# Kernel optimization log

Measured on AMD Instinct MI355X. Metric: run time of the kernel, lower is better.

Reference implementation:

```python
import jax, jax.numpy as jnp
import numpy as np

N_QUBITS = 8
N_LAYERS = 4
N_WIRES = N_QUBITS + 1  # circuit uses an extra ancilla wire
B = 16384
D = 512
LN_EPS = 1e-5


def _rx(theta):
    # RX(t) = [[cos(t/2), -i sin(t/2)], [-i sin(t/2), cos(t/2)]]; theta: () or (B,)
    c = jnp.cos(theta / 2).astype(jnp.complex64)
    s = (-1j) * jnp.sin(theta / 2).astype(jnp.complex64)
    return jnp.stack([jnp.stack([c, s], -1), jnp.stack([s, c], -1)], -2)


def _ry(theta):
    c = jnp.cos(theta / 2).astype(jnp.complex64)
    s = jnp.sin(theta / 2).astype(jnp.complex64)
    return jnp.stack([jnp.stack([c, -s], -1), jnp.stack([s, c], -1)], -2)


def _rz(theta):
    # RZ(t) = diag(e^{-it/2}, e^{it/2})
    half = (theta / 2).astype(jnp.complex64)
    em = jnp.exp(-1j * half)
    ep = jnp.exp(1j * half)
    z = jnp.zeros_like(em)
    return jnp.stack([jnp.stack([em, z], -1), jnp.stack([z, ep], -1)], -2)


def _apply_1q(state, U, wire):
    # state: (B,) + (2,)*N_WIRES ; U: (2,2) shared or (B,2,2) per-sample
    ax = 1 + wire
    s = jnp.moveaxis(state, ax, -1)
    if U.ndim == 2:
        s = jnp.einsum('ij,...j->...i', U, s)
    else:
        s = jnp.einsum('bij,b...j->b...i', U, s)
    return jnp.moveaxis(s, -1, ax)


def _cnot(state, c, t):
    # flip target wire t on the control=1 slice of wire c
    s = jnp.moveaxis(state, (1 + c, 1 + t), (-2, -1))
    s = jnp.stack([s[..., 0, :], jnp.flip(s[..., 1, :], axis=-1)], axis=-2)
    return jnp.moveaxis(s, (-2, -1), (1 + c, 1 + t))


def _quantum_circuit(angles, q_weights):
    # angles: (B, N_QUBITS) per-sample data angles; q_weights: (N_LAYERS, N_QUBITS+1)
    b = angles.shape[0]
    state = jnp.zeros((b, 2 ** N_WIRES), jnp.complex64).at[:, 0].set(1.0)
    state = state.reshape((b,) + (2,) * N_WIRES)
    # data encoding: RX, RZ with per-sample angles
    for i in range(N_QUBITS):
        state = _apply_1q(state, _rx(angles[:, i]), i)
        state = _apply_1q(state, _rz(angles[:, i]), i)
    # first variational layer
    for i in range(N_QUBITS):
        state = _apply_1q(state, _rx(q_weights[0, i]), i)
        state = _apply_1q(state, _rz(q_weights[1, i]), i)
    # entangling layers
    for l in range(1, N_LAYERS):
        for i in range(N_QUBITS):
            state = _cnot(state, i, (i + 1) % N_QUBITS)
            state = _apply_1q(state, _ry(q_weights[l, i]), i)
            state = _apply_1q(state, _rz(q_weights[l, i]), i)
        state = _cnot(state, N_QUBITS - 1, N_QUBITS)
        state = _apply_1q(state, _ry(q_weights[l, -1]), N_QUBITS)
    probs = state.real ** 2 + state.imag ** 2
    # <Z_i> = P(q_i=0) - P(q_i=1)
    zs = []
    for i in range(N_QUBITS):
        axes = tuple(1 + j for j in range(N_WIRES) if j != i)
        p = probs.sum(axes)  # (B, 2)
        zs.append(p[:, 0] - p[:, 1])
    return jnp.stack(zs, axis=1)  # (B, N_QUBITS)


def _forward(x, timestep, w_in, b_in, ln_gamma, ln_beta, q_weights, w_out, b_out):
    h = jnp.tanh(x @ w_in.T + b_in)  # (B, 8)
    mu = h.mean(-1, keepdims=True)
    var = ((h - mu) ** 2).mean(-1, keepdims=True)
    h = (h - mu) / jnp.sqrt(var + LN_EPS) * ln_gamma + ln_beta
    angles = h + timestep  # broadcast scalar timestep
    q_out = _quantum_circuit(angles, q_weights)
    out = q_out @ w_out.T + b_out
    return x + out  # input_dim == output_dim -> residual


def setup_inputs() -> dict:
    key = jax.random.key(0)
    ks = jax.random.split(key, 6)
    x = jax.random.normal(ks[0], (B, D), jnp.float32)
    timestep = jax.random.uniform(ks[1], (1,), jnp.float32)
    w_in = jax.random.normal(ks[2], (N_QUBITS, D), jnp.float32) * np.float32(1.0 / np.sqrt(D))
    b_in = jnp.zeros((N_QUBITS,), jnp.float32)
    ln_gamma = jnp.ones((N_QUBITS,), jnp.float32)
    ln_beta = jnp.zeros((N_QUBITS,), jnp.float32)
    q_weights = jax.random.uniform(ks[3], (N_LAYERS, N_QUBITS + 1), jnp.float32, 0.0, 2.0 * np.pi)
    w_out = jax.random.normal(ks[4], (D, N_QUBITS), jnp.float32) * np.float32(1.0 / np.sqrt(N_QUBITS))
    b_out = jnp.zeros((D,), jnp.float32)
    return {'x': x, 'timestep': timestep, 'w_in': w_in, 'b_in': b_in,
            'ln_gamma': ln_gamma, 'ln_beta': ln_beta, 'q_weights': q_weights,
            'w_out': w_out, 'b_out': b_out}


def reference(x, timestep, w_in, b_in, ln_gamma, ln_beta, q_weights, w_out, b_out):
    return _forward(x, timestep, w_in, b_in, ln_gamma, ln_beta, q_weights, w_out, b_out)
```

## Files before the change

### kernel.cpp

```cpp
#include <hip/hip_runtime.h>
#include <math.h>

#define NSAMP 16384
#define ND    512

typedef float f2 __attribute__((ext_vector_type(2)));
__device__ __forceinline__ f2 spl(float x) { return (f2){x, x}; }

template<int CTRL>
__device__ __forceinline__ float dppf(float x) {
  return __int_as_float(__builtin_amdgcn_update_dpp(
      __float_as_int(x), __float_as_int(x), CTRL, 0xF, 0xF, true));
}
template<int CTRL, int RM, int BM>
__device__ __forceinline__ float dppf_keep(float x) {
  return __int_as_float(__builtin_amdgcn_update_dpp(
      __float_as_int(x), __float_as_int(x), CTRL, RM, BM, false));
}
template<int P>
__device__ __forceinline__ float swzf(float x) {
  return __int_as_float(__builtin_amdgcn_ds_swizzle(__float_as_int(x), P));
}

#if __has_builtin(__builtin_amdgcn_permlane16_swap)
#define HAVE_PLSWAP 1
#endif
__device__ __forceinline__ void plswap16(float x, float& a, float& b) {
#ifdef HAVE_PLSWAP
  auto r = __builtin_amdgcn_permlane16_swap(__float_as_uint(x), __float_as_uint(x), false, false);
  a = __uint_as_float(r[0]); b = __uint_as_float(r[1]);
#else
  a = x; b = swzf<0x401F>(x);
#endif
}
__device__ __forceinline__ void plswap32(float x, float& a, float& b) {
#ifdef HAVE_PLSWAP
  auto r = __builtin_amdgcn_permlane32_swap(__float_as_uint(x), __float_as_uint(x), false, false);
  a = __uint_as_float(r[0]); b = __uint_as_float(r[1]);
#else
  a = x; b = __shfl_xor(x, 32, 64);
#endif
}

template<int M>
__device__ __forceinline__ f2 bfly2(f2 x) {
  f2 r;
  if constexpr (M == 1)       { r.x = dppf<0xB1>(x.x);    r.y = dppf<0xB1>(x.y); }
  else if constexpr (M == 2)  { r.x = dppf<0x4E>(x.x);    r.y = dppf<0x4E>(x.y); }
  else if constexpr (M == 8)  { r.x = dppf<0x128>(x.x);   r.y = dppf<0x128>(x.y); }
  else if constexpr (M == 4)  { r.x = swzf<0x101F>(x.x);  r.y = swzf<0x101F>(x.y); }
  else if constexpr (M == 16) { r.x = swzf<0x401F>(x.x);  r.y = swzf<0x401F>(x.y); }
  else                        { r.x = __shfl_xor(x.x, 32, 64); r.y = __shfl_xor(x.y, 32, 64); }
  return r;
}

__device__ __forceinline__ float fold8_allsum(const float* y, int lane) {
  float v4[4];
#pragma unroll
  for (int i = 0; i < 4; ++i) {
    float keep = (lane & 1) ? y[2 * i + 1] : y[2 * i];
    float send = (lane & 1) ? y[2 * i]     : y[2 * i + 1];
    v4[i] = keep + dppf<0xB1>(send);
  }
  float v2[2];
#pragma unroll
  for (int i = 0; i < 2; ++i) {
    float keep = (lane & 2) ? v4[2 * i + 1] : v4[2 * i];
    float send = (lane & 2) ? v4[2 * i]     : v4[2 * i + 1];
    v2[i] = keep + dppf<0x4E>(send);
  }
  float keep = (lane & 4) ? v2[1] : v2[0];
  float send = (lane & 4) ? v2[0] : v2[1];
  float r = keep + swzf<0x101F>(send);
  r += dppf<0x128>(r);
  { float a, b; plswap16(r, a, b); r = a + b; }
  { float a, b; plswap32(r, a, b); r = a + b; }
  return r;
}

__device__ __forceinline__ float grp8_sum(float x) {
  x += dppf<0xB1>(x);
  x += dppf<0x4E>(x);
  x += swzf<0x101F>(x);
  return x;
}

__device__ __forceinline__ f2 cmul(f2 a, f2 b) {
  f2 bs = __builtin_shufflevector(b, b, 1, 0);
  f2 t  = (f2){-a.y, a.y} * bs;
  return spl(a.x) * b + t;
}

template<int LB>
__device__ __forceinline__ void ry_local(f2* s, float c, float sv) {
#pragma unroll
  for (int r0 = 0; r0 < 8; ++r0) {
    if (r0 & (1 << LB)) continue;
    const int r1 = r0 | (1 << LB);
    f2 a0 = s[r0], a1 = s[r1];
    s[r0] = spl(c) * a0 - spl(sv) * a1;
    s[r1] = spl(sv) * a0 + spl(c) * a1;
  }
}
template<int LB>
__device__ __forceinline__ void rz_local(f2* s, f2 phm, f2 php) {
#pragma unroll
  for (int r = 0; r < 8; ++r) s[r] = cmul(s[r], (r & (1 << LB)) ? php : phm);
}
template<int M>
__device__ __forceinline__ void ry_lane(f2* s, float c, float se) {
#pragma unroll
  for (int r = 0; r < 8; ++r) {
    f2 p = bfly2<M>(s[r]);
    s[r] = spl(c) * s[r] + spl(se) * p;
  }
}
template<int CB, int TB>
__device__ __forceinline__ void cnot_ll(f2* s) {
#pragma unroll
  for (int r0 = 0; r0 < 8; ++r0) {
    if (!(r0 & (1 << CB)) || (r0 & (1 << TB))) continue;
    const int r1 = r0 | (1 << TB);
    f2 t = s[r0]; s[r0] = s[r1]; s[r1] = t;
  }
}
template<int CB, int TM>
__device__ __forceinline__ void cnot_lt(f2* s) {
#pragma unroll
  for (int r = 0; r < 8; ++r) {
    if (!(r & (1 << CB))) continue;
    s[r] = bfly2<TM>(s[r]);
  }
}
template<int CM, int TM>
__device__ __forceinline__ void cnot_tt(f2* s, bool cc) {
#pragma unroll
  for (int r = 0; r < 8; ++r) {
    f2 p = bfly2<TM>(s[r]);
    s[r].x = cc ? p.x : s[r].x;
    s[r].y = cc ? p.y : s[r].y;
  }
}
__device__ __forceinline__ void cnot_m4_t1(f2* s) {
#pragma unroll
  for (int r = 0; r < 8; ++r) {
    s[r].x = dppf_keep<0xB1, 0xF, 0xA>(s[r].x);
    s[r].y = dppf_keep<0xB1, 0xF, 0xA>(s[r].y);
  }
}
__device__ __forceinline__ void cnot_m1_t2(f2* s) {
#pragma unroll
  for (int r = 0; r < 8; ++r) {
    s[r].x = dppf<0x6C>(s[r].x);
    s[r].y = dppf<0x6C>(s[r].y);
  }
}
template<int TB>
__device__ __forceinline__ void cnot_tl(f2* s, bool cc) {
#pragma unroll
  for (int r0 = 0; r0 < 8; ++r0) {
    if (r0 & (1 << TB)) continue;
    const int r1 = r0 | (1 << TB);
    f2 n0, n1;
    n0.x = cc ? s[r1].x : s[r0].x;  n0.y = cc ? s[r1].y : s[r0].y;
    n1.x = cc ? s[r0].x : s[r1].x;  n1.y = cc ? s[r0].y : s[r1].y;
    s[r0] = n0; s[r1] = n1;
  }
}

__global__ void qpre_kernel(const float* __restrict__ qw, float* __restrict__ ws) {
  int t = threadIdx.x;
  if (t < 27) {
    float s, c; __sincosf(qw[9 + t] * 0.5f, &s, &c);
    ws[2 * t] = c; ws[2 * t + 1] = s;
  }
}

template<bool PRE>
struct Consts {
  const float* qw; const float* ws;
  __device__ __forceinline__ f2 ltrig(int l, int i) const {
    if constexpr (PRE) {
      return ((const f2*)ws)[(l - 1) * 9 + i];
    } else {
      float s, c; __sincosf(qw[l * 9 + i] * 0.5f, &s, &c);
      return (f2){c, s};
    }
  }
};

template<bool PRE, bool FULL>
__device__ __forceinline__ void do_layer(f2* st, int lane, const Consts<PRE>& cst, int l) {
  f2 t[9];
#pragma unroll
  for (int i = 0; i < 9; ++i) t[i] = cst.ltrig(l, i);

  cnot_ll<0, 1>(st);
  ry_local<0>(st, t[0].x, t[0].y);
  rz_local<0>(st, (f2){t[0].x, -t[0].y}, (f2){t[0].x, t[0].y});
  cnot_ll<1, 2>(st);
  ry_local<1>(st, t[1].x, t[1].y);
  cnot_lt<2, 4>(st);
  ry_local<2>(st, t[2].x, t[2].y);
  cnot_m4_t1(st);
  { float se = (lane & 4) ? t[3].y : -t[3].y;
    ry_lane<4>(st, t[3].x, se); }
  cnot_m1_t2(st);
  { float se = (lane & 1) ? t[4].y : -t[4].y;
    ry_lane<1>(st, t[4].x, se); }
  cnot_tt<2, 8>(st, (lane & 2) != 0);
  { float se = (lane & 2) ? t[5].y : -t[5].y;
    ry_lane<2>(st, t[5].x, se); }
  cnot_tt<8, 16>(st, (lane & 8) != 0);
  { float se = (lane & 8) ? t[6].y : -t[6].y;
    ry_lane<8>(st, t[6].x, se); }
  cnot_tl<0>(st, (lane & 16) != 0);
  { float se = (lane & 16) ? t[7].y : -t[7].y;
    ry_lane<16>(st, t[7].x, se); }

  if constexpr (FULL) {
    cnot_tt<16, 32>(st, (lane & 16) != 0);
    { float se = (lane & 32) ? t[8].y : -t[8].y;
      ry_lane<32>(st, t[8].x, se); }
    f2 L4[4];
#pragma unroll
    for (int k = 0; k < 4; ++k) {
      f2 p1 = (f2){t[1].x, (k & 1) ? t[1].y : -t[1].y};
      f2 p2 = (f2){t[2].x, (k & 2) ? t[2].y : -t[2].y};
      L4[k] = cmul(p1, p2);
    }
    f2 phW = (f2){t[3].x, (lane & 4)  ? t[3].y : -t[3].y};
    phW = cmul(phW, (f2){t[4].x, (lane & 1)  ? t[4].y : -t[4].y});
    phW = cmul(phW, (f2){t[5].x, (lane & 2)  ? t[5].y : -t[5].y});
    phW = cmul(phW, (f2){t[6].x, (lane & 8)  ? t[6].y : -t[6].y});
    phW = cmul(phW, (f2){t[7].x, (lane & 16) ? t[7].y : -t[7].y});
    f2 pr[4];
#pragma unroll
    for (int k = 0; k < 4; ++k) pr[k] = cmul(L4[k], phW);
#pragma unroll
    for (int r = 0; r < 8; ++r) st[r] = cmul(st[r], pr[(r >> 1) & 3]);
  }
}

template<bool PRE>
__global__ __launch_bounds__(256, 4) void qlayer_kernel(
    const float* __restrict__ x, const float* __restrict__ tstep,
    const float* __restrict__ w_in, const float* __restrict__ b_in,
    const float* __restrict__ g, const float* __restrict__ be,
    const float* __restrict__ qw, const float* __restrict__ w_out,
    const float* __restrict__ b_out, float* __restrict__ out,
    const float* __restrict__ ws)
{
  __shared__ float4 s_w4v[1024];
  __shared__ __align__(16) float s_u[4][8][4];
  __shared__ __align__(16) float s_z[4][8];
  float* s_w4 = (float*)s_w4v;

  const int tid = threadIdx.x;
#pragma unroll
  for (int k = 0; k < 16; ++k) {
    int e = tid + 256 * k;
    int j = e >> 9, d = e & 511;
    s_w4[(j >> 2) * 2048 + d * 4 + (j & 3)] = w_in[e];
  }
  __syncthreads();

  const int lane   = tid & 63;
  const int wv     = tid >> 6;
  const int sample = blockIdx.x * 4 + wv;
  const int jq     = lane & 7;

  const float* xrow = x + (size_t)sample * ND;
  float xv[8];
#pragma unroll
  for (int m = 0; m < 8; ++m) xv[m] = xrow[lane + 64 * m];

  f2 hA = (f2){0.f, 0.f}, hB = hA, hC = hA, hD = hA;
  const float4* w4 = (const float4*)s_w4v;
#pragma unroll
  for (int m = 0; m < 8; ++m) {
    const int d = lane + 64 * m;
    float4 w0 = w4[d];
    float4 w1 = w4[512 + d];
    f2 xm = spl(xv[m]);
    hA += xm * (f2){w0.x, w0.y};  hB += xm * (f2){w0.z, w0.w};
    hC += xm * (f2){w1.x, w1.y};  hD += xm * (f2){w1.z, w1.w};
  }
  float h[8] = {hA.x, hA.y, hB.x, hB.y, hC.x, hC.y, hD.x, hD.y};
  const float H = fold8_allsum(h, lane);

  const float t0 = tstep[0];
  float tj;
  {
    float v = H + b_in[jq];
    v = fminf(15.f, fmaxf(-15.f, v));
    float e2 = __expf(2.f * v);
    tj = (e2 - 1.f) * __builtin_amdgcn_rcpf(e2 + 1.f);
  }
  const float mu = grp8_sum(tj) * 0.125f;
  const float dv = tj - mu;
  const float var = grp8_sum(dv * dv) * 0.125f;
  const float rstd = rsqrtf(var + 1e-5f);
  const float ang = dv * rstd * g[jq] + be[jq] + t0;

  {
    float sa, ca; __sincosf(ang * 0.5f, &sa, &ca);
    f2 v0 = spl(ca) * (f2){ca, -sa};
    f2 v1 = spl(sa) * (f2){sa, -ca};
    float s0, c0, s1, c1;
    __sincosf(qw[jq] * 0.5f, &s0, &c0);
    __sincosf(qw[9 + jq] * 0.5f, &s1, &c1);
    f2 M00 = (f2){ c1 * c0, -s1 * c0};
    f2 M01 = (f2){-s1 * s0, -c1 * s0};
    f2 M10 = (f2){ s1 * s0, -c1 * s0};
    f2 M11 = (f2){ c1 * c0,  s1 * c0};
    f2 u0 = cmul(M00, v0) + cmul(M01, v1);
    f2 u1 = cmul(M10, v0) + cmul(M11, v1);
    if (lane < 8) {
      float4 uu = {u0.x, u0.y, u1.x, u1.y};
      *(float4*)&s_u[wv][jq][0] = uu;
    }
  }
  asm volatile("s_waitcnt lgkmcnt(0)" ::: "memory");
  __builtin_amdgcn_sched_barrier(0);

  f2 u0a[3], u1a[3];
#pragma unroll
  for (int i = 0; i < 3; ++i) {
    float4 uu = *(const float4*)&s_u[wv][i][0];
    u0a[i] = (f2){uu.x, uu.y};
    u1a[i] = (f2){uu.z, uu.w};
  }
  f2 hl;
  {
    const f2* ub = (const f2*)&s_u[wv][0][0];
    f2 r4 = ub[4 * 2 + ((lane >> 0) & 1)];
    f2 r5 = ub[5 * 2 + ((lane >> 1) & 1)];
    f2 r3 = ub[3 * 2 + ((lane >> 2) & 1)];
    f2 r6 = ub[6 * 2 + ((lane >> 3) & 1)];
    f2 r7 = ub[7 * 2 + ((lane >> 4) & 1)];
    hl = cmul(cmul(cmul(cmul(r4, r5), r3), r6), r7);
    if (lane & 32) hl = (f2){0.f, 0.f};
  }
  f2 t01[4];
#pragma unroll
  for (int q = 0; q < 4; ++q)
    t01[q] = cmul((q & 1) ? u1a[0] : u0a[0], (q & 2) ? u1a[1] : u0a[1]);
  f2 st[8];
#pragma unroll
  for (int r = 0; r < 8; ++r)
    st[r] = cmul(cmul(t01[r & 3], (r & 4) ? u1a[2] : u0a[2]), hl);

  Consts<PRE> cst{qw, ws};
  do_layer<PRE, true >(st, lane, cst, 1);
  do_layer<PRE, true >(st, lane, cst, 2);
  do_layer<PRE, false>(st, lane, cst, 3);

  float p[8];
#pragma unroll
  for (int r = 0; r < 8; ++r) p[r] = st[r].x * st[r].x + st[r].y * st[r].y;
  float tot = 0.f;
#pragma unroll
  for (int r = 0; r < 8; ++r) tot += p[r];

  float y[8];
  y[0] = (p[0] - p[1]) + (p[2] - p[3]) + (p[4] - p[5]) + (p[6] - p[7]);
  y[1] = (p[0] + p[1]) - (p[2] + p[3]) + (p[4] + p[5]) - (p[6] + p[7]);
  y[2] = (p[0] + p[1] + p[2] + p[3]) - (p[4] + p[5] + p[6] + p[7]);
  y[3] = (lane & 4)  ? -tot : tot;
  y[4] = (lane & 1)  ? -tot : tot;
  y[5] = (lane & 2)  ? -tot : tot;
  y[6] = (lane & 8)  ? -tot : tot;
  y[7] = (lane & 16) ? -tot : tot;
  const float Z = fold8_allsum(y, lane);
  if (lane < 8) s_z[wv][jq] = Z;
  asm volatile("s_waitcnt lgkmcnt(0)" ::: "memory");
  __builtin_amdgcn_sched_barrier(0);

  float4 za = *(const float4*)&s_z[wv][0];
  float4 zb = *(const float4*)&s_z[wv][4];

  const size_t base = (size_t)sample * ND;
  const float4* wo4 = (const float4*)w_out;
  f2 z01 = (f2){za.x, za.y}, z23 = (f2){za.z, za.w};
  f2 z45 = (f2){zb.x, zb.y}, z67 = (f2){zb.z, zb.w};
#pragma unroll
  for (int m = 0; m < 8; ++m) {
    const int d = lane + 64 * m;
    float4 a  = wo4[2 * d];
    float4 b4 = wo4[2 * d + 1];
    f2 acc = z01 * (f2){a.x, a.y};
    acc += z23 * (f2){a.z, a.w};
    acc += z45 * (f2){b4.x, b4.y};
    acc += z67 * (f2){b4.z, b4.w};
    out[base + d] = xv[m] + b_out[d] + acc.x + acc.y;
  }
}

extern "C" void kernel_launch(void* const* d_in, const int* in_sizes, int n_in,
                              void* d_out, int out_size, void* d_ws, size_t ws_size,
                              hipStream_t stream) {
  const float* x     = (const float*)d_in[0];
  const float* ts    = (const float*)d_in[1];
  const float* w_in  = (const float*)d_in[2];
  const float* b_in  = (const float*)d_in[3];
  const float* g     = (const float*)d_in[4];
  const float* be    = (const float*)d_in[5];
  const float* qw    = (const float*)d_in[6];
  const float* w_out = (const float*)d_in[7];
  const float* b_out = (const float*)d_in[8];
  float* out = (float*)d_out;

  const bool pre = (d_ws != nullptr) && (ws_size >= 256);
  if (pre) {
    qpre_kernel<<<dim3(1), dim3(64), 0, stream>>>(qw, (float*)d_ws);
    qlayer_kernel<true><<<dim3(NSAMP / 4), dim3(256), 0, stream>>>(
        x, ts, w_in, b_in, g, be, qw, w_out, b_out, out, (const float*)d_ws);
  } else {
    qlayer_kernel<false><<<dim3(NSAMP / 4), dim3(256), 0, stream>>>(
        x, ts, w_in, b_in, g, be, qw, w_out, b_out, out, (const float*)d_ws);
  }
}
```

Measured before the change: 58.46 us.

## Drop LDS w_in staging, use contiguous per-lane vector loads and bpermute CNOTs

Removes the per-block LDS transpose of w_in and its __syncthreads. Each lane now reads 8 contiguous x, w_in, w_out and b_out elements as float4 and writes its output as float4. The conditional butterfly CNOTs become single ds_bpermute permutations. The ancilla-wire handling is restructured: the state starts nonzero in the upper half-wave, the layer-1 ancilla CNOT+RY is folded into a per-lane scalar multiply, and layer 2 uses a bpermute. This cuts LDS traffic and select work, but w_in is now read from global or cache by every wave, and the new ancilla math changes numerics and carries some correctness risk.

```diff
diff --git a/kernel.cpp b/kernel.cpp
--- a/kernel.cpp
+++ b/kernel.cpp
@@ -20,6 +20,9 @@
 template<int P>
 __device__ __forceinline__ float swzf(float x) {
   return __int_as_float(__builtin_amdgcn_ds_swizzle(__float_as_int(x), P));
+}
+__device__ __forceinline__ float bpermf(int addrB, float x) {
+  return __int_as_float(__builtin_amdgcn_ds_bpermute(addrB, __float_as_int(x)));
 }
 
 #if __has_builtin(__builtin_amdgcn_permlane16_swap)
@@ -132,13 +135,11 @@
     s[r] = bfly2<TM>(s[r]);
   }
 }
-template<int CM, int TM>
-__device__ __forceinline__ void cnot_tt(f2* s, bool cc) {
+__device__ __forceinline__ void cnot_bperm(f2* s, int addrB) {
 #pragma unroll
   for (int r = 0; r < 8; ++r) {
-    f2 p = bfly2<TM>(s[r]);
-    s[r].x = cc ? p.x : s[r].x;
-    s[r].y = cc ? p.y : s[r].y;
+    s[r].x = bpermf(addrB, s[r].x);
+    s[r].y = bpermf(addrB, s[r].y);
   }
 }
 __device__ __forceinline__ void cnot_m4_t1(f2* s) {
@@ -189,8 +190,9 @@
   }
 };
 
-template<bool PRE, bool FULL>
-__device__ __forceinline__ void do_layer(f2* st, int lane, const Consts<PRE>& cst, int l) {
+template<bool PRE, int MODE>
+__device__ __forceinline__ void do_layer(f2* st, int lane, const Consts<PRE>& cst, int l,
+                                         int addr56, int addr67, int addr78) {
   f2 t[9];
 #pragma unroll
   for (int i = 0; i < 9; ++i) t[i] = cst.ltrig(l, i);
@@ -208,20 +210,26 @@
   cnot_m1_t2(st);
   { float se = (lane & 1) ? t[4].y : -t[4].y;
     ry_lane<1>(st, t[4].x, se); }
-  cnot_tt<2, 8>(st, (lane & 2) != 0);
+  cnot_bperm(st, addr56);
   { float se = (lane & 2) ? t[5].y : -t[5].y;
     ry_lane<2>(st, t[5].x, se); }
-  cnot_tt<8, 16>(st, (lane & 8) != 0);
+  cnot_bperm(st, addr67);
   { float se = (lane & 8) ? t[6].y : -t[6].y;
     ry_lane<8>(st, t[6].x, se); }
   cnot_tl<0>(st, (lane & 16) != 0);
   { float se = (lane & 16) ? t[7].y : -t[7].y;
     ry_lane<16>(st, t[7].x, se); }
 
-  if constexpr (FULL) {
-    cnot_tt<16, 32>(st, (lane & 16) != 0);
-    { float se = (lane & 32) ? t[8].y : -t[8].y;
-      ry_lane<32>(st, t[8].x, se); }
+  if constexpr (MODE == 1) {
+    const float wsel = (lane & 32) ? ((lane & 16) ? t[8].x : t[8].y)
+                                   : ((lane & 16) ? -t[8].y : t[8].x);
+#pragma unroll
+    for (int r = 0; r < 8; ++r) st[r] = st[r] * spl(wsel);
+  }
+  if constexpr (MODE == 2) {
+    cnot_bperm(st, addr78);
+  }
+  if constexpr (MODE != 3) {
     f2 L4[4];
 #pragma unroll
     for (int k = 0; k < 4; ++k) {
@@ -251,42 +259,36 @@
     const float* __restrict__ b_out, float* __restrict__ out,
     const float* __restrict__ ws)
 {
-  __shared__ float4 s_w4v[1024];
   __shared__ __align__(16) float s_u[4][8][4];
   __shared__ __align__(16) float s_z[4][8];
-  float* s_w4 = (float*)s_w4v;
-
-  const int tid = threadIdx.x;
-#pragma unroll
-  for (int k = 0; k < 16; ++k) {
-    int e = tid + 256 * k;
-    int j = e >> 9, d = e & 511;
-    s_w4[(j >> 2) * 2048 + d * 4 + (j & 3)] = w_in[e];
-  }
-  __syncthreads();
-
+
+  const int tid    = threadIdx.x;
   const int lane   = tid & 63;
   const int wv     = tid >> 6;
   const int sample = blockIdx.x * 4 + wv;
   const int jq     = lane & 7;
-
-  const float* xrow = x + (size_t)sample * ND;
-  float xv[8];
-#pragma unroll
-  for (int m = 0; m < 8; ++m) xv[m] = xrow[lane + 64 * m];
-
-  f2 hA = (f2){0.f, 0.f}, hB = hA, hC = hA, hD = hA;
-  const float4* w4 = (const float4*)s_w4v;
-#pragma unroll
-  for (int m = 0; m < 8; ++m) {
-    const int d = lane + 64 * m;
-    float4 w0 = w4[d];
-    float4 w1 = w4[512 + d];
-    f2 xm = spl(xv[m]);
-    hA += xm * (f2){w0.x, w0.y};  hB += xm * (f2){w0.z, w0.w};
-    hC += xm * (f2){w1.x, w1.y};  hD += xm * (f2){w1.z, w1.w};
-  }
-  float h[8] = {hA.x, hA.y, hB.x, hB.y, hC.x, hC.y, hD.x, hD.y};
+  const int dbase  = lane << 3;
+
+  const int addr56 = (lane ^ ((lane & 2) << 2)) << 2;
+  const int addr67 = (lane ^ ((lane & 8) << 1)) << 2;
+  const int addr78 = (lane ^ ((lane & 16) << 1)) << 2;
+
+  const float4* xr4 = (const float4*)(x + (size_t)sample * ND + dbase);
+  const float4 xa = xr4[0], xb = xr4[1];
+  const f2 xp0 = (f2){xa.x, xa.y}, xp1 = (f2){xa.z, xa.w};
+  const f2 xp2 = (f2){xb.x, xb.y}, xp3 = (f2){xb.z, xb.w};
+
+  float h[8];
+#pragma unroll
+  for (int j = 0; j < 8; ++j) {
+    const float4* wj = (const float4*)(w_in + j * ND + dbase);
+    float4 wa = wj[0], wb = wj[1];
+    f2 acc = xp0 * (f2){wa.x, wa.y};
+    acc += xp1 * (f2){wa.z, wa.w};
+    acc += xp2 * (f2){wb.x, wb.y};
+    acc += xp3 * (f2){wb.z, wb.w};
+    h[j] = acc.x + acc.y;
+  }
   const float H = fold8_allsum(h, lane);
 
   const float t0 = tstep[0];
@@ -340,7 +342,6 @@
     f2 r6 = ub[6 * 2 + ((lane >> 3) & 1)];
     f2 r7 = ub[7 * 2 + ((lane >> 4) & 1)];
     hl = cmul(cmul(cmul(cmul(r4, r5), r3), r6), r7);
-    if (lane & 32) hl = (f2){0.f, 0.f};
   }
   f2 t01[4];
 #pragma unroll
@@ -352,9 +353,9 @@
     st[r] = cmul(cmul(t01[r & 3], (r & 4) ? u1a[2] : u0a[2]), hl);
 
   Consts<PRE> cst{qw, ws};
-  do_layer<PRE, true >(st, lane, cst, 1);
-  do_layer<PRE, true >(st, lane, cst, 2);
-  do_layer<PRE, false>(st, lane, cst, 3);
+  do_layer<PRE, 1>(st, lane, cst, 1, addr56, addr67, addr78);
+  do_layer<PRE, 2>(st, lane, cst, 2, addr56, addr67, addr78);
+  do_layer<PRE, 3>(st, lane, cst, 3, addr56, addr67, addr78);
 
   float p[8];
 #pragma unroll
@@ -380,21 +381,27 @@
   float4 za = *(const float4*)&s_z[wv][0];
   float4 zb = *(const float4*)&s_z[wv][4];
 
-  const size_t base = (size_t)sample * ND;
-  const float4* wo4 = (const float4*)w_out;
-  f2 z01 = (f2){za.x, za.y}, z23 = (f2){za.z, za.w};
-  f2 z45 = (f2){zb.x, zb.y}, z67 = (f2){zb.z, zb.w};
-#pragma unroll
-  for (int m = 0; m < 8; ++m) {
-    const int d = lane + 64 * m;
-    float4 a  = wo4[2 * d];
-    float4 b4 = wo4[2 * d + 1];
-    f2 acc = z01 * (f2){a.x, a.y};
-    acc += z23 * (f2){a.z, a.w};
-    acc += z45 * (f2){b4.x, b4.y};
-    acc += z67 * (f2){b4.z, b4.w};
-    out[base + d] = xv[m] + b_out[d] + acc.x + acc.y;
-  }
+  const f2 z01 = (f2){za.x, za.y}, z23 = (f2){za.z, za.w};
+  const f2 z45 = (f2){zb.x, zb.y}, z67 = (f2){zb.z, zb.w};
+  const float4* wo = (const float4*)(w_out + (size_t)dbase * 8);
+  const float4* bo = (const float4*)(b_out + dbase);
+  const float4 b0 = bo[0], b1 = bo[1];
+  const float xk[8] = {xa.x, xa.y, xa.z, xa.w, xb.x, xb.y, xb.z, xb.w};
+  const float bk[8] = {b0.x, b0.y, b0.z, b0.w, b1.x, b1.y, b1.z, b1.w};
+  float o[8];
+#pragma unroll
+  for (int k = 0; k < 8; ++k) {
+    float4 wa = wo[2 * k];
+    float4 wb = wo[2 * k + 1];
+    f2 acc = z01 * (f2){wa.x, wa.y};
+    acc += z23 * (f2){wa.z, wa.w};
+    acc += z45 * (f2){wb.x, wb.y};
+    acc += z67 * (f2){wb.z, wb.w};
+    o[k] = xk[k] + bk[k] + acc.x + acc.y;
+  }
+  float4* outp = (float4*)(out + (size_t)sample * ND + dbase);
+  outp[0] = (float4){o[0], o[1], o[2], o[3]};
+  outp[1] = (float4){o[4], o[5], o[6], o[7]};
 }
 
 extern "C" void kernel_launch(void* const* d_in, const int* in_sizes, int n_in,
```

Result: no change. 58.18 us (-0.5%).
